# Optimization experiments

Hardware: AMD Instinct MI355X
Metric: run time of the kernel (lower is better)

## Reference

```python
import jax, jax.numpy as jnp
import numpy as np


def setup_inputs() -> dict:
    key = jax.random.key(0)
    k1, k2, k3 = jax.random.split(key, 3)
    B, C, H, W = 64, 256, 32, 32   # batch, hidden_dim, latent grid
    D, K = 128, 1024               # latent_dim, num_embeddings
    z = jax.random.normal(k1, (B, C, H, W), dtype=jnp.float32)
    proj_w = jax.random.normal(k2, (D, C), dtype=jnp.float32) * 0.02  # 1x1 conv kernel [out,in]
    proj_b = jnp.zeros((D,), jnp.float32)
    # codebook init uniform(-1/K, 1/K) as in torch module
    embed = (jax.random.uniform(k3, (K, D), dtype=jnp.float32) * 2.0 - 1.0) / K
    return {"z": z, "proj_w": proj_w, "proj_b": proj_b, "embed": embed}


def reference(z, proj_w, proj_b, embed):
    # 1x1 conv projection: [B,C,H,W] -> [B,H,W,D]  (fuses conv + permute)
    zp = jnp.einsum('bchw,dc->bhwd', z, proj_w) + proj_b
    B, H, W, D = zp.shape
    zf = zp.reshape(-1, D)                                   # [N, D], N = B*H*W
    # squared Euclidean distance to codebook: ||z||^2 - 2 z.e + ||e||^2  -> [N, K]
    dist = (jnp.sum(zf * zf, axis=1, keepdims=True)
            - 2.0 * (zf @ embed.T)
            + jnp.sum(embed * embed, axis=1))
    min_indices = jnp.argmin(dist, axis=1)                   # [N]
    z_q = embed[min_indices].reshape(B, H, W, D)             # codebook gather
    # straight-through estimator
    rep_z_q = zp + jax.lax.stop_gradient(z_q - zp)
    rep_z_q = rep_z_q.transpose(0, 3, 1, 2)                  # back to NCHW
    return rep_z_q, min_indices
```

## Files before the change

### kernel.cpp

```cpp
#include <hip/hip_runtime.h>

#define B_   64
#define C_   256
#define D_   128
#define HW_  1024
#define K_   1024
#define N_   65536
#define MARGIN_PREF 1.2e-3f

typedef __attribute__((ext_vector_type(8))) short short8;
typedef __attribute__((ext_vector_type(4))) float f32x4;

__device__ __forceinline__ unsigned short f2bf(float f) {
    unsigned u = __float_as_uint(f);
    return (unsigned short)((u + 0x7FFFu + ((u >> 16) & 1u)) >> 16);
}
__device__ __forceinline__ unsigned long long packdk(float d, int k) {
    unsigned u = __float_as_uint(d);
    u = (u & 0x80000000u) ? ~u : (u | 0x80000000u);
    return ((unsigned long long)u << 10) | (unsigned)k;
}
__device__ __forceinline__ float unpackd(unsigned long long key) {
    unsigned u = (unsigned)(key >> 10);
    u = (u & 0x80000000u) ? (u ^ 0x80000000u) : ~u;
    return __uint_as_float(u);
}
__device__ __forceinline__ unsigned long long min64(unsigned long long a, unsigned long long b) {
    return a < b ? a : b;
}

template <typename F>
__device__ __forceinline__ float np_sum128(F ld) {
#pragma clang fp contract(off)
    float r0 = ld(0), r1 = ld(1), r2 = ld(2), r3 = ld(3);
    float r4 = ld(4), r5 = ld(5), r6 = ld(6), r7 = ld(7);
#pragma unroll
    for (int i = 8; i < 128; i += 8) {
        r0 = r0 + ld(i + 0); r1 = r1 + ld(i + 1);
        r2 = r2 + ld(i + 2); r3 = r3 + ld(i + 3);
        r4 = r4 + ld(i + 4); r5 = r5 + ld(i + 5);
        r6 = r6 + ld(i + 6); r7 = r7 + ld(i + 7);
    }
    return ((r0 + r1) + (r2 + r3)) + ((r4 + r5) + (r6 + r7));
}

__global__ __launch_bounds__(256) void k0_norms(const float* __restrict__ embed,
                                                float* __restrict__ enorm,
                                                unsigned short* __restrict__ ebf) {
#pragma clang fp contract(off)
    int k = blockIdx.x * 256 + threadIdx.x;
    if (k >= K_) return;
    const float* e = embed + (size_t)k * D_;
    enorm[k] = np_sum128([&](int i) { float v = e[i]; return v * v; });
#pragma unroll 8
    for (int i = 0; i < 128; ++i) ebf[(size_t)k * 128 + i] = f2bf(e[i]);
}

__global__ __launch_bounds__(256) void k1_proj(const float* __restrict__ z,
                                               const float* __restrict__ w,
                                               const float* __restrict__ bias,
                                               float* __restrict__ zp,
                                               unsigned short* __restrict__ zbf) {
#pragma clang fp contract(off)
    __shared__ float zs[64][64];
    __shared__ float wsh[64][128];
    const int b   = blockIdx.x >> 4;
    const int hw0 = (blockIdx.x & 15) << 6;
    const int t   = threadIdx.x;
    const int hwg = (t & 7) * 8;
    const int dg  = (t >> 3) * 4;

    float acc[8][4];
#pragma unroll
    for (int i = 0; i < 8; ++i)
#pragma unroll
        for (int j = 0; j < 4; ++j) acc[i][j] = 0.f;

    for (int ct = 0; ct < C_; ct += 64) {
        __syncthreads();
#pragma unroll
        for (int i = 0; i < 16; ++i) {
            int idx = i * 256 + t;
            int cc = idx >> 6, hwl = idx & 63;
            zs[cc][hwl] = z[(((size_t)b * C_ + ct + cc) << 10) + hw0 + hwl];
        }
#pragma unroll
        for (int i = 0; i < 32; ++i) {
            int idx = i * 256 + t;
            int cc = idx >> 7, d = idx & 127;
            wsh[cc][d] = w[(size_t)d * C_ + ct + cc];
        }
        __syncthreads();
#pragma unroll 2
        for (int cc = 0; cc < 64; ++cc) {
            float4 za = *(const float4*)&zs[cc][hwg];
            float4 zb = *(const float4*)&zs[cc][hwg + 4];
            float4 wv = *(const float4*)&wsh[cc][dg];
            float zv[8]  = {za.x, za.y, za.z, za.w, zb.x, zb.y, zb.z, zb.w};
            float wva[4] = {wv.x, wv.y, wv.z, wv.w};
#pragma unroll
            for (int i = 0; i < 8; ++i)
#pragma unroll
                for (int j = 0; j < 4; ++j) {
                    float p = zv[i] * wva[j];
                    acc[i][j] = acc[i][j] + p;
                }
        }
    }
#pragma unroll
    for (int i = 0; i < 8; ++i)
#pragma unroll
        for (int j = 0; j < 4; ++j) {
            float v = acc[i][j] + bias[dg + j];
            size_t off = (((size_t)b * HW_ + hw0 + hwg + i) << 7) + dg + j;
            zp[off]  = v;
            zbf[off] = f2bf(v);
        }
}

__global__ __launch_bounds__(256) void k0z_znorm(const float* __restrict__ zp,
                                                 float* __restrict__ znorm) {
#pragma clang fp contract(off)
    __shared__ float zl[64][129];
    const int t = threadIdx.x, n0 = blockIdx.x * 64;
#pragma unroll
    for (int i = 0; i < 32; ++i) {
        int idx = i * 256 + t;
        zl[idx >> 7][idx & 127] = zp[(size_t)n0 * 128 + idx];
    }
    __syncthreads();
    if (t < 64)
        znorm[n0 + t] = np_sum128([&](int i) { float v = zl[t][i]; return v * v; });
}

__global__ __launch_bounds__(256) void k2_argmin(const unsigned short* __restrict__ zbf,
                                                 const unsigned short* __restrict__ ebf,
                                                 const float* __restrict__ zp,
                                                 const float* __restrict__ embed,
                                                 const float* __restrict__ enorm,
                                                 const float* __restrict__ znorm,
                                                 int* __restrict__ bestk_ws,
                                                 float* __restrict__ out_idx) {
    __shared__ unsigned char etile[32 * 272];
    const int t   = threadIdx.x;
    const int l   = t & 63;
    const int wid = t >> 6;
    const int r0  = (blockIdx.x * 4 + wid) * 16;
    const int lr  = l & 15;
    const int lh  = l >> 4;

    short8 zfrag[4];
#pragma unroll
    for (int dt = 0; dt < 4; ++dt)
        zfrag[dt] = *(const short8*)(zbf + (((size_t)(r0 + lr)) << 7) + dt * 32 + lh * 8);

    const int srow = t >> 4, scol = t & 15;

    unsigned long long bk = ~0ull;
#pragma unroll 1
    for (int st = 0; st < 32; ++st) {
        __syncthreads();
#pragma unroll
        for (int i = 0; i < 2; ++i) {
            int row = i * 16 + srow;
            *(short8*)(etile + row * 272 + scol * 16) =
                *(const short8*)(ebf + (((size_t)(st * 32 + row)) << 7) + scol * 8);
        }
        __syncthreads();
#pragma unroll
        for (int ks = 0; ks < 2; ++ks) {
            short8 af[4];
#pragma unroll
            for (int dt = 0; dt < 4; ++dt)
                af[dt] = *(const short8*)(etile + (ks * 16 + lr) * 272 + dt * 64 + lh * 16);
            f32x4 en4 = *(const f32x4*)(enorm + st * 32 + ks * 16 + lh * 4);
            f32x4 acc = {0.f, 0.f, 0.f, 0.f};
#pragma unroll
            for (int dt = 0; dt < 4; ++dt)
                acc = __builtin_amdgcn_mfma_f32_16x16x32_bf16(af[dt], zfrag[dt], acc, 0, 0, 0);
#pragma unroll
            for (int reg = 0; reg < 4; ++reg) {
                float dist = fmaf(-2.f, acc[reg], en4[reg]);
                bk = min64(bk, packdk(dist, st * 32 + ks * 16 + lh * 4 + reg));
            }
        }
    }
    {
        unsigned long long o;
        o = __shfl_xor(bk, 16, 64); bk = min64(bk, o);
        o = __shfl_xor(bk, 32, 64); bk = min64(bk, o);
    }
    const float thr = unpackd(bk) + MARGIN_PREF;

    unsigned long long ca = 0, cb = 0;
    int cnt = 0;
#pragma unroll 1
    for (int st = 0; st < 32; ++st) {
        __syncthreads();
#pragma unroll
        for (int i = 0; i < 2; ++i) {
            int row = i * 16 + srow;
            *(short8*)(etile + row * 272 + scol * 16) =
                *(const short8*)(ebf + (((size_t)(st * 32 + row)) << 7) + scol * 8);
        }
        __syncthreads();
#pragma unroll
        for (int ks = 0; ks < 2; ++ks) {
            short8 af[4];
#pragma unroll
            for (int dt = 0; dt < 4; ++dt)
                af[dt] = *(const short8*)(etile + (ks * 16 + lr) * 272 + dt * 64 + lh * 16);
            f32x4 en4 = *(const f32x4*)(enorm + st * 32 + ks * 16 + lh * 4);
            f32x4 acc = {0.f, 0.f, 0.f, 0.f};
#pragma unroll
            for (int dt = 0; dt < 4; ++dt)
                acc = __builtin_amdgcn_mfma_f32_16x16x32_bf16(af[dt], zfrag[dt], acc, 0, 0, 0);
#pragma unroll
            for (int reg = 0; reg < 4; ++reg) {
                float dist = fmaf(-2.f, acc[reg], en4[reg]);
                if (dist < thr) {
                    int kk = st * 32 + ks * 16 + lh * 4 + reg;
                    if (cnt < 6)       ca |= (unsigned long long)kk << (10 * cnt);
                    else if (cnt < 12) cb |= (unsigned long long)kk << (10 * (cnt - 6));
                    ++cnt;
                }
            }
        }
    }

    const int myrow = r0 + lr;
    const float* zrow = zp + ((size_t)myrow << 7);
    const float  zn   = znorm[myrow];
    unsigned long long best = ~0ull;

    auto refine = [&](int kk) {
#pragma clang fp contract(off)
        const float* e = embed + ((size_t)kk << 7);
        float s = 0.f;
#pragma unroll 1
        for (int d = 0; d < 128; ++d) s = fmaf(zrow[d], e[d], s);
        float T  = 2.0f * s;
        float A  = zn - T;
        float Bv = A + enorm[kk];
        best = min64(best, packdk(Bv, kk));
    };

    if (cnt <= 12) {
#pragma unroll
        for (int i = 0; i < 6; ++i)
            if (i < cnt) refine((int)((ca >> (10 * i)) & 1023ull));
#pragma unroll
        for (int i = 6; i < 12; ++i)
            if (i < cnt) refine((int)((cb >> (10 * (i - 6))) & 1023ull));
    } else {
#pragma unroll 1
        for (int kt = 0; kt < 64; ++kt)
#pragma unroll
            for (int reg = 0; reg < 4; ++reg) refine(kt * 16 + lh * 4 + reg);
    }
    {
        unsigned long long o;
        o = __shfl_xor(best, 16, 64); best = min64(best, o);
        o = __shfl_xor(best, 32, 64); best = min64(best, o);
    }
    if (l < 16) {
        int kk = (int)(best & 1023ull);
        bestk_ws[r0 + l] = kk;
        out_idx[r0 + l]  = (float)kk;
    }
}

__global__ __launch_bounds__(256) void k3_gather(const float* __restrict__ embed,
                                                 const int* __restrict__ bestk,
                                                 float* __restrict__ out0) {
    __shared__ float tile[64][129];
    const int b   = blockIdx.x >> 4;
    const int hw0 = (blockIdx.x & 15) << 6;
    const int t   = threadIdx.x;
    const int n0  = b * HW_ + hw0;
#pragma unroll
    for (int i = 0; i < 32; ++i) {
        int idx = i * 256 + t;
        int hwl = idx >> 7, d = idx & 127;
        int k = bestk[n0 + hwl];
        tile[hwl][d] = embed[(size_t)k * 128 + d];
    }
    __syncthreads();
#pragma unroll
    for (int i = 0; i < 32; ++i) {
        int idx = i * 256 + t;
        int d = idx >> 6, hwl = idx & 63;
        out0[(((size_t)b * D_ + d) << 10) + hw0 + hwl] = tile[hwl][d];
    }
}

extern "C" void kernel_launch(void* const* d_in, const int* in_sizes, int n_in,
                              void* d_out, int out_size, void* d_ws, size_t ws_size,
                              hipStream_t stream) {
    const float* z     = (const float*)d_in[0];
    const float* pw    = (const float*)d_in[1];
    const float* pb    = (const float*)d_in[2];
    const float* embed = (const float*)d_in[3];

    float* out0 = (float*)d_out;
    float* out1 = (float*)d_out + (size_t)B_ * D_ * HW_;

    char* ws = (char*)d_ws;
    float*          zp    = (float*)ws;
    unsigned short* zbf   = (unsigned short*)(ws + (32u << 20));
    unsigned short* ebf   = (unsigned short*)(ws + (48u << 20));
    float*          enorm = (float*)(ws + (48u << 20) + (256u << 10));
    float*          znorm = (float*)(ws + (49u << 20));
    int*            bestk = (int*)  (ws + (50u << 20));

    hipLaunchKernelGGL(k0_norms,  dim3(4),    dim3(256), 0, stream, embed, enorm, ebf);
    hipLaunchKernelGGL(k1_proj,   dim3(1024), dim3(256), 0, stream, z, pw, pb, zp, zbf);
    hipLaunchKernelGGL(k0z_znorm, dim3(1024), dim3(256), 0, stream, zp, znorm);
    hipLaunchKernelGGL(k2_argmin, dim3(1024), dim3(256), 0, stream,
                       zbf, ebf, zp, embed, enorm, znorm, bestk, out1);
    hipLaunchKernelGGL(k3_gather, dim3(1024), dim3(256), 0, stream, embed, bestk, out0);
}
```

Before: 390.3 us.

## Double-buffer codebook tiles via direct global-to-LDS loads with pre-swizzled layout

The argmin kernel no longer copies each codebook tile through registers into LDS between two barriers. It now issues asynchronous global_load_lds transfers of the next tile into a second LDS buffer while the current tile is being used for MFMA work, which removes one barrier per step. The norms kernel now stores the bf16 codebook with a row-dependent XOR swizzle and vectorized writes, so a plain linear copy into LDS gives bank-conflict-free fragment reads without padding. The cost is twice the LDS per block and a reliance on the barrier to wait for the async loads. Any other reader of the bf16 codebook must also understand the swizzled layout.

```diff
diff --git a/kernel.cpp b/kernel.cpp
--- a/kernel.cpp
+++ b/kernel.cpp
@@ -52,8 +52,15 @@
     if (k >= K_) return;
     const float* e = embed + (size_t)k * D_;
     enorm[k] = np_sum128([&](int i) { float v = e[i]; return v * v; });
-#pragma unroll 8
-    for (int i = 0; i < 128; ++i) ebf[(size_t)k * 128 + i] = f2bf(e[i]);
+    const int sw = (k & 7) << 4;
+    char* rowp = (char*)ebf + ((size_t)k << 8);
+#pragma unroll
+    for (int j = 0; j < 16; ++j) {
+        short8 v;
+#pragma unroll
+        for (int q = 0; q < 8; ++q) v[q] = (short)f2bf(e[j * 8 + q]);
+        *(short8*)(rowp + ((j * 16) ^ sw)) = v;
+    }
 }
 
 __global__ __launch_bounds__(256) void k1_proj(const float* __restrict__ z,
@@ -141,7 +148,7 @@
                                                  const float* __restrict__ znorm,
                                                  int* __restrict__ bestk_ws,
                                                  float* __restrict__ out_idx) {
-    __shared__ unsigned char etile[32 * 272];
+    __shared__ unsigned char etile[2][32 * 256];
     const int t   = threadIdx.x;
     const int l   = t & 63;
     const int wid = t >> 6;
@@ -154,25 +161,39 @@
     for (int dt = 0; dt < 4; ++dt)
         zfrag[dt] = *(const short8*)(zbf + (((size_t)(r0 + lr)) << 7) + dt * 32 + lh * 8);
 
-    const int srow = t >> 4, scol = t & 15;
+    const int swz = (lr & 7) << 4;
+    int roff[4];
+#pragma unroll
+    for (int dt = 0; dt < 4; ++dt)
+        roff[dt] = lr * 256 + ((dt * 64 + lh * 16) ^ swz);
+
+    const char* ebf_b   = (const char*)ebf;
+    const int   stg_off = wid * 1024;
+
+    auto STAGE = [&](int st, int b) {
+#pragma unroll
+        for (int j = 0; j < 2; ++j) {
+            int off = j * 4096 + stg_off;
+            __builtin_amdgcn_global_load_lds(
+                (const __attribute__((address_space(1))) void*)(ebf_b + ((size_t)st << 13) + off + (l << 4)),
+                (__attribute__((address_space(3))) void*)(&etile[b][off]),
+                16, 0, 0);
+        }
+    };
 
     unsigned long long bk = ~0ull;
+    STAGE(0, 0);
 #pragma unroll 1
     for (int st = 0; st < 32; ++st) {
         __syncthreads();
-#pragma unroll
-        for (int i = 0; i < 2; ++i) {
-            int row = i * 16 + srow;
-            *(short8*)(etile + row * 272 + scol * 16) =
-                *(const short8*)(ebf + (((size_t)(st * 32 + row)) << 7) + scol * 8);
-        }
-        __syncthreads();
+        if (st < 31) STAGE(st + 1, (st + 1) & 1);
+        const unsigned char* buf = etile[st & 1];
 #pragma unroll
         for (int ks = 0; ks < 2; ++ks) {
             short8 af[4];
 #pragma unroll
             for (int dt = 0; dt < 4; ++dt)
-                af[dt] = *(const short8*)(etile + (ks * 16 + lr) * 272 + dt * 64 + lh * 16);
+                af[dt] = *(const short8*)(buf + ks * 4096 + roff[dt]);
             f32x4 en4 = *(const f32x4*)(enorm + st * 32 + ks * 16 + lh * 4);
             f32x4 acc = {0.f, 0.f, 0.f, 0.f};
 #pragma unroll
@@ -194,22 +215,19 @@
 
     unsigned long long ca = 0, cb = 0;
     int cnt = 0;
+    __syncthreads();
+    STAGE(0, 0);
 #pragma unroll 1
     for (int st = 0; st < 32; ++st) {
         __syncthreads();
-#pragma unroll
-        for (int i = 0; i < 2; ++i) {
-            int row = i * 16 + srow;
-            *(short8*)(etile + row * 272 + scol * 16) =
-                *(const short8*)(ebf + (((size_t)(st * 32 + row)) << 7) + scol * 8);
-        }
-        __syncthreads();
+        if (st < 31) STAGE(st + 1, (st + 1) & 1);
+        const unsigned char* buf = etile[st & 1];
 #pragma unroll
         for (int ks = 0; ks < 2; ++ks) {
             short8 af[4];
 #pragma unroll
             for (int dt = 0; dt < 4; ++dt)
-                af[dt] = *(const short8*)(etile + (ks * 16 + lr) * 272 + dt * 64 + lh * 16);
+                af[dt] = *(const short8*)(buf + ks * 4096 + roff[dt]);
             f32x4 en4 = *(const f32x4*)(enorm + st * 32 + ks * 16 + lh * 4);
             f32x4 acc = {0.f, 0.f, 0.f, 0.f};
 #pragma unroll
```

After: 386.2 us. No clear change (-1.1%).
